# Performance work log

Measured on AMD Instinct MI355X. Metric: run time of the kernel, lower is better.

Reference implementation:

```python
import jax, jax.numpy as jnp
import numpy as np

MODEL_DIM = 1024
NUM_HEADS = 16
DIM_PER_HEAD = MODEL_DIM // NUM_HEADS
LN_EPS = 1e-5


def setup_inputs() -> dict:
    key = jax.random.key(0)
    ks = jax.random.split(key, 12)
    B, L, D = 4, 2048, MODEL_DIM
    s = 0.02
    return {
        "query": jax.random.normal(ks[0], (B, L, D), jnp.float32),
        "key": jax.random.normal(ks[1], (B, L, D), jnp.float32),
        "value": jax.random.normal(ks[2], (B, L, D), jnp.float32),
        "Wq": jax.random.normal(ks[3], (D, D), jnp.float32) * s,
        "bq": jnp.zeros((D,), jnp.float32),
        "Wk": jax.random.normal(ks[4], (D, D), jnp.float32) * s,
        "bk": jnp.zeros((D,), jnp.float32),
        "Wv": jax.random.normal(ks[5], (D, D), jnp.float32) * s,
        "bv": jnp.zeros((D,), jnp.float32),
        "Wo": jax.random.normal(ks[6], (D, D), jnp.float32) * s,
        "bo": jnp.zeros((D,), jnp.float32),
        "gamma": jnp.ones((D,), jnp.float32),
        "beta": jnp.zeros((D,), jnp.float32),
    }


def reference(query, key, value, Wq, bq, Wk, bk, Wv, bv, Wo, bo, gamma, beta):
    B, L, D = query.shape
    H, d = NUM_HEADS, DIM_PER_HEAD
    scale = d ** (-0.5)
    # torch nn.Linear: y = x @ W.T + b
    q = (query @ Wq.T + bq).reshape(B * H, L, d)  # faithful row-major view split
    k = (key @ Wk.T + bk).reshape(B * H, L, d)
    v = (value @ Wv.T + bv).reshape(B * H, L, d)
    atten = jnp.einsum('bqd,bkd->bqk', q, k) * scale  # [B*H, L, L]
    atten = jax.nn.softmax(atten, axis=2)
    # dropout: identity in eval mode
    context = jnp.einsum('bqk,bkd->bqd', atten, v).reshape(B, L, D)
    output = context @ Wo.T + bo
    x = query + output  # residual
    mu = jnp.mean(x, axis=-1, keepdims=True)
    var = jnp.var(x, axis=-1, keepdims=True)
    out = (x - mu) * jax.lax.rsqrt(var + LN_EPS) * gamma + beta
    return (out, atten)
```

## Files before the change

### kernel.cpp

```cpp
#include <hip/hip_runtime.h>
#include <cstdint>
#include <cstddef>

typedef _Float16 half8 __attribute__((ext_vector_type(8)));
typedef _Float16 half4 __attribute__((ext_vector_type(4)));
typedef __fp16 fp16x2 __attribute__((ext_vector_type(2)));
typedef float f32x4 __attribute__((ext_vector_type(4)));
typedef int int2v __attribute__((ext_vector_type(2)));

#define MFMA16(a, b, c) __builtin_amdgcn_mfma_f32_16x16x32_f16((a), (b), (c), 0, 0, 0)
#define MFMA16x16(a, b, c) __builtin_amdgcn_mfma_f32_16x16x16f16((a), (b), (c), 0, 0, 0)

__device__ __forceinline__ void gload_lds16(const void* g, void* l) {
  __builtin_amdgcn_global_load_lds(
      (const __attribute__((address_space(1))) void*)g,
      (__attribute__((address_space(3))) void*)l, 16, 0, 0);
}

__device__ __forceinline__ float fexp2(float x) {
#if __has_builtin(__builtin_amdgcn_exp2f)
  return __builtin_amdgcn_exp2f(x);
#else
  return exp2f(x);
#endif
}

__device__ __forceinline__ int cvtpk16(float a, float b) {
  fp16x2 h = __builtin_amdgcn_cvt_pkrtz(a, b);
  return __builtin_bit_cast(int, h);
}

__global__ __launch_bounds__(256) void cvt_f16(
    const float* __restrict__ q, const float* __restrict__ k, const float* __restrict__ v,
    const float* __restrict__ wq, const float* __restrict__ wk, const float* __restrict__ wv,
    _Float16* __restrict__ xq, _Float16* __restrict__ xk, _Float16* __restrict__ xv,
    _Float16* __restrict__ wq16, _Float16* __restrict__ wk16, _Float16* __restrict__ wv16)
{
  constexpr int S8 = 1048576;
  constexpr int W8 = 131072;
  int u = blockIdx.x * 256 + threadIdx.x;
  const float* src;
  _Float16* dst;
  if (u < S8) { src = q; dst = xq; }
  else if ((u -= S8) < S8) { src = k; dst = xk; }
  else if ((u -= S8) < S8) { src = v; dst = xv; }
  else if ((u -= S8) < W8) { src = wq; dst = wq16; }
  else if ((u -= W8) < W8) { src = wk; dst = wk16; }
  else { u -= W8; src = wv; dst = wv16; }
  const float4 f0 = reinterpret_cast<const float4*>(src)[u * 2];
  const float4 f1 = reinterpret_cast<const float4*>(src)[u * 2 + 1];
  half8 h;
  h[0] = (_Float16)f0.x; h[1] = (_Float16)f0.y; h[2] = (_Float16)f0.z; h[3] = (_Float16)f0.w;
  h[4] = (_Float16)f1.x; h[5] = (_Float16)f1.y; h[6] = (_Float16)f1.z; h[7] = (_Float16)f1.w;
  reinterpret_cast<half8*>(dst)[u] = h;
}

__global__ __launch_bounds__(256) void vtrans(
    const _Float16* __restrict__ v, _Float16* __restrict__ vt)
{
  __shared__ _Float16 T[64][72];
  const int g = blockIdx.y, kt = blockIdx.x;
  const int tid = threadIdx.x;
  const size_t gbase = (size_t)g * 131072;
  const int sr = tid >> 2, sc = (tid & 3) * 16;
  {
    const half8* src = reinterpret_cast<const half8*>(v + gbase + (size_t)(kt * 64 + sr) * 64 + sc);
    *reinterpret_cast<half8*>(&T[sr][sc]) = src[0];
    *reinterpret_cast<half8*>(&T[sr][sc + 8]) = src[1];
  }
  __syncthreads();
  const int d = tid >> 2, kc = (tid & 3) * 16;
  half8 h0, h1;
#pragma unroll
  for (int j = 0; j < 8; ++j) { h0[j] = T[kc + j][d]; h1[j] = T[kc + 8 + j][d]; }
  half8* dst = reinterpret_cast<half8*>(vt + gbase + (size_t)d * 2048 + kt * 64 + kc);
  dst[0] = h0;
  dst[1] = h1;
}

template <bool WF32, bool RES>
__global__ __launch_bounds__(256) void gemm128(
    const _Float16* __restrict__ A, const void* __restrict__ Wp,
    const float* __restrict__ bias, const float* __restrict__ resid,
    void* __restrict__ Out, int N, float scale)
{
  constexpr int K = 1024;
  __shared__ _Float16 As[128 * 64];
  __shared__ _Float16 Bs[128 * 64];
  const int tid = threadIdx.x;
  const int lane = tid & 63, w = tid >> 6;
  const int lo = lane & 15, hi = lane >> 4;
  const int wr = w >> 1, wc = w & 1;
  const int rbase = blockIdx.x * 128, cbase = blockIdx.y * 128;
  const int e0 = w * 512 + lane * 8;

  f32x4 acc[4][4];
#pragma unroll
  for (int m = 0; m < 4; ++m)
#pragma unroll
    for (int n = 0; n < 4; ++n) acc[m][n] = f32x4{0.f, 0.f, 0.f, 0.f};

  for (int kk = 0; kk < K; kk += 64) {
    __syncthreads();
#pragma unroll
    for (int i = 0; i < 4; ++i) {
      const int e = i * 2048 + e0;
      gload_lds16(A + (size_t)(rbase + (e >> 6)) * K + kk + (e & 63),
                  (char*)As + i * 4096 + w * 1024);
    }
    if constexpr (!WF32) {
#pragma unroll
      for (int i = 0; i < 4; ++i) {
        const int e = i * 2048 + e0;
        gload_lds16((const _Float16*)Wp + (size_t)(cbase + (e >> 6)) * K + kk + (e & 63),
                    (char*)Bs + i * 4096 + w * 1024);
      }
    } else {
#pragma unroll
      for (int i = 0; i < 4; ++i) {
        const int e = i * 2048 + e0;
        const float4* src = reinterpret_cast<const float4*>(
            (const float*)Wp + (size_t)(cbase + (e >> 6)) * K + kk + (e & 63));
        const float4 f0 = src[0], f1 = src[1];
        half8 h;
        h[0] = (_Float16)f0.x; h[1] = (_Float16)f0.y; h[2] = (_Float16)f0.z; h[3] = (_Float16)f0.w;
        h[4] = (_Float16)f1.x; h[5] = (_Float16)f1.y; h[6] = (_Float16)f1.z; h[7] = (_Float16)f1.w;
        *reinterpret_cast<half8*>(Bs + e) = h;
      }
    }
    __syncthreads();
#pragma unroll
    for (int k0 = 0; k0 < 2; ++k0) {
      half8 a[4], b[4];
#pragma unroll
      for (int m = 0; m < 4; ++m)
        a[m] = *reinterpret_cast<const half8*>(As + (wr * 64 + m * 16 + lo) * 64 + k0 * 32 + hi * 8);
#pragma unroll
      for (int n = 0; n < 4; ++n)
        b[n] = *reinterpret_cast<const half8*>(Bs + (wc * 64 + n * 16 + lo) * 64 + k0 * 32 + hi * 8);
#pragma unroll
      for (int m = 0; m < 4; ++m)
#pragma unroll
        for (int n = 0; n < 4; ++n) acc[m][n] = MFMA16(a[m], b[n], acc[m][n]);
    }
  }
#pragma unroll
  for (int m = 0; m < 4; ++m) {
#pragma unroll
    for (int n = 0; n < 4; ++n) {
      const int col = cbase + wc * 64 + n * 16 + lo;
      const float bv = bias[col];
#pragma unroll
      for (int r = 0; r < 4; ++r) {
        const int row = rbase + wr * 64 + m * 16 + hi * 4 + r;
        float v = acc[m][n][r] + bv;
        if constexpr (RES) {
          v += resid[(size_t)row * 1024 + col];
          ((float*)Out)[(size_t)row * N + col] = v;
        } else {
          ((_Float16*)Out)[(size_t)row * N + col] = (_Float16)(v * scale);
        }
      }
    }
  }
}

__global__ __launch_bounds__(512) void attn_fused(
    const _Float16* __restrict__ qg, const _Float16* __restrict__ kg,
    const _Float16* __restrict__ vtg, _Float16* __restrict__ ctx,
    float* __restrict__ attnp)
{
  __shared__ _Float16 Kt[2][64 * 64];
  __shared__ _Float16 Vt[2][64 * 64];
  __shared__ float Ps[8 * 1024];
  const int tid = threadIdx.x;
  const int lane = tid & 63, w = tid >> 6;
  const int lo = lane & 15, hi = lane >> 4;
  const int bid = blockIdx.x;
  const int g = bid & 63;
  const int q0 = (bid >> 6) * 256;
  const size_t gbase = (size_t)g * (2048 * 64);
  const int e0 = tid * 8;

  const int r0 = e0 >> 6, c0 = (e0 & 63) ^ ((r0 & 7) << 3);

  half8 q[2][2];
#pragma unroll
  for (int m = 0; m < 2; ++m)
#pragma unroll
    for (int k0 = 0; k0 < 2; ++k0)
      q[m][k0] = *reinterpret_cast<const half8*>(
          qg + gbase + (size_t)(q0 + w * 32 + m * 16 + lo) * 64 + k0 * 32 + hi * 8);

  float ls[2] = {0.f, 0.f};

  gload_lds16(kg + gbase + (size_t)r0 * 64 + c0, (char*)Kt[0] + w * 1024);

  for (int kt = 0; kt < 32; ++kt) {
    const int cur = kt & 1;
    __syncthreads();
    if (kt < 31) {
      const _Float16* kn = kg + gbase + (size_t)(kt + 1) * (64 * 64);
      gload_lds16(kn + (size_t)r0 * 64 + c0, (char*)Kt[cur ^ 1] + w * 1024);
    }
    f32x4 s[2][4];
#pragma unroll
    for (int m = 0; m < 2; ++m)
#pragma unroll
      for (int n = 0; n < 4; ++n) s[m][n] = f32x4{0.f, 0.f, 0.f, 0.f};
#pragma unroll
    for (int k0 = 0; k0 < 2; ++k0) {
      half8 b[4];
#pragma unroll
      for (int n = 0; n < 4; ++n) {
        const int row = n * 16 + lo;
        b[n] = *reinterpret_cast<const half8*>(
            Kt[cur] + row * 64 + ((k0 * 32 + hi * 8) ^ ((row & 7) << 3)));
      }
#pragma unroll
      for (int m = 0; m < 2; ++m)
#pragma unroll
        for (int n = 0; n < 4; ++n) s[m][n] = MFMA16(b[n], q[m][k0], s[m][n]);
    }
#pragma unroll
    for (int m = 0; m < 2; ++m) {
      float t = 0.f;
#pragma unroll
      for (int nb = 0; nb < 4; ++nb)
#pragma unroll
        for (int r = 0; r < 4; ++r) t += fexp2(s[m][nb][r]);
      ls[m] += t;
    }
  }

  float dr[2];
#pragma unroll
  for (int m = 0; m < 2; ++m) {
    float t = ls[m];
    t += __shfl_xor(t, 16, 64);
    t += __shfl_xor(t, 32, 64);
    dr[m] = __log2f(t);
  }

  f32x4 o[2][4];
#pragma unroll
  for (int m = 0; m < 2; ++m)
#pragma unroll
    for (int n = 0; n < 4; ++n) o[m][n] = f32x4{0.f, 0.f, 0.f, 0.f};
  float* ab = attnp + (size_t)g * 2048 * 2048;
  const _Float16* vtb = vtg + (size_t)g * (64 * 2048);

  gload_lds16(kg + gbase + (size_t)r0 * 64 + c0, (char*)Kt[0] + w * 1024);
  gload_lds16(vtb + (size_t)r0 * 2048 + c0, (char*)Vt[0] + w * 1024);

  for (int kt = 0; kt < 32; ++kt) {
    const int cur = kt & 1;
    if (kt == 0) asm volatile("s_waitcnt vmcnt(0) lgkmcnt(0)" ::: "memory");
    else asm volatile("s_waitcnt vmcnt(8) lgkmcnt(0)" ::: "memory");
    __builtin_amdgcn_s_barrier();
    __builtin_amdgcn_sched_barrier(0);
    if (kt < 31) {
      const _Float16* kn = kg + gbase + (size_t)(kt + 1) * (64 * 64);
      const _Float16* vn = vtb + (kt + 1) * 64;
      gload_lds16(kn + (size_t)r0 * 64 + c0, (char*)Kt[cur ^ 1] + w * 1024);
      gload_lds16(vn + (size_t)r0 * 2048 + c0, (char*)Vt[cur ^ 1] + w * 1024);
    }
    __builtin_amdgcn_sched_barrier(0);
    f32x4 s[2][4];
#pragma unroll
    for (int m = 0; m < 2; ++m)
#pragma unroll
      for (int n = 0; n < 4; ++n)
        s[m][n] = f32x4{-dr[m], -dr[m], -dr[m], -dr[m]};
#pragma unroll
    for (int k0 = 0; k0 < 2; ++k0) {
      half8 b[4];
#pragma unroll
      for (int n = 0; n < 4; ++n) {
        const int row = n * 16 + lo;
        b[n] = *reinterpret_cast<const half8*>(
            Kt[cur] + row * 64 + ((k0 * 32 + hi * 8) ^ ((row & 7) << 3)));
      }
#pragma unroll
      for (int m = 0; m < 2; ++m)
#pragma unroll
        for (int n = 0; n < 4; ++n) s[m][n] = MFMA16(b[n], q[m][k0], s[m][n]);
    }
    int pk[2][4][2];
    float* Pw = Ps + w * 1024;
#pragma unroll
    for (int m = 0; m < 2; ++m) {
#pragma unroll
      for (int nb = 0; nb < 4; ++nb) {
        const float p0 = fexp2(s[m][nb][0]);
        const float p1 = fexp2(s[m][nb][1]);
        const float p2 = fexp2(s[m][nb][2]);
        const float p3 = fexp2(s[m][nb][3]);
        pk[m][nb][0] = cvtpk16(p0, p1);
        pk[m][nb][1] = cvtpk16(p2, p3);
        const f32x4 f = {p0, p1, p2, p3};
        *reinterpret_cast<f32x4*>(
            Pw + lo * 64 + ((nb * 16 + hi * 4) ^ ((lo & 15) << 2))) = f;
      }
      asm volatile("s_waitcnt lgkmcnt(0)" ::: "memory");
#pragma unroll
      for (int i = 0; i < 4; ++i) {
        const int rl = i * 4 + (lane >> 4);
        const int klo = (lane & 15) * 4;
        const f32x4 f = *reinterpret_cast<const f32x4*>(
            Pw + rl * 64 + (klo ^ ((rl & 15) << 2)));
        __builtin_nontemporal_store(
            f, reinterpret_cast<f32x4*>(
                   ab + (size_t)(q0 + w * 32 + m * 16 + rl) * 2048 + kt * 64 + klo));
      }
      asm volatile("s_waitcnt lgkmcnt(0)" ::: "memory");
    }
#pragma unroll
    for (int nb = 0; nb < 4; ++nb) {
      half4 vb[4];
#pragma unroll
      for (int n = 0; n < 4; ++n) {
        const int d = n * 16 + lo;
        vb[n] = *reinterpret_cast<const half4*>(
            Vt[cur] + d * 64 + ((nb * 16 + hi * 4) ^ ((d & 7) << 3)));
      }
#pragma unroll
      for (int m = 0; m < 2; ++m) {
        const int2v t = {pk[m][nb][0], pk[m][nb][1]};
        const half4 pa = __builtin_bit_cast(half4, t);
#pragma unroll
        for (int n = 0; n < 4; ++n) o[m][n] = MFMA16x16(pa, vb[n], o[m][n]);
      }
    }
  }
#pragma unroll
  for (int m = 0; m < 2; ++m)
#pragma unroll
    for (int n = 0; n < 4; ++n)
#pragma unroll
      for (int r = 0; r < 4; ++r)
        ctx[gbase + (size_t)(q0 + w * 32 + m * 16 + hi * 4 + r) * 64 + n * 16 + lo] =
            (_Float16)o[m][n][r];
}

__global__ __launch_bounds__(256) void ln_kernel(
    float* __restrict__ x, const float* __restrict__ gamma, const float* __restrict__ beta)
{
  const int row = blockIdx.x;
  const int t = threadIdx.x;
  float4 v = *reinterpret_cast<float4*>(x + (size_t)row * 1024 + t * 4);
  float s = v.x + v.y + v.z + v.w;
  float ss = v.x * v.x + v.y * v.y + v.z * v.z + v.w * v.w;
#pragma unroll
  for (int off = 1; off < 64; off <<= 1) {
    s += __shfl_xor(s, off, 64);
    ss += __shfl_xor(ss, off, 64);
  }
  __shared__ float sm[8];
  const int wv = t >> 6, ln = t & 63;
  if (ln == 0) { sm[wv] = s; sm[4 + wv] = ss; }
  __syncthreads();
  s = sm[0] + sm[1] + sm[2] + sm[3];
  ss = sm[4] + sm[5] + sm[6] + sm[7];
  const float mu = s * (1.0f / 1024.0f);
  const float var = ss * (1.0f / 1024.0f) - mu * mu;
  const float rstd = rsqrtf(var + 1e-5f);
  const float4 gv = *reinterpret_cast<const float4*>(gamma + t * 4);
  const float4 bv = *reinterpret_cast<const float4*>(beta + t * 4);
  v.x = (v.x - mu) * rstd * gv.x + bv.x;
  v.y = (v.y - mu) * rstd * gv.y + bv.y;
  v.z = (v.z - mu) * rstd * gv.z + bv.z;
  v.w = (v.w - mu) * rstd * gv.w + bv.w;
  *reinterpret_cast<float4*>(x + (size_t)row * 1024 + t * 4) = v;
}

extern "C" void kernel_launch(void* const* d_in, const int* in_sizes, int n_in,
                              void* d_out, int out_size, void* d_ws, size_t ws_size,
                              hipStream_t stream) {
  const float* query = (const float*)d_in[0];
  const float* key_ = (const float*)d_in[1];
  const float* value = (const float*)d_in[2];
  const float* Wq = (const float*)d_in[3];
  const float* bq = (const float*)d_in[4];
  const float* Wk = (const float*)d_in[5];
  const float* bk = (const float*)d_in[6];
  const float* Wv = (const float*)d_in[7];
  const float* bv = (const float*)d_in[8];
  const float* Wo = (const float*)d_in[9];
  const float* bo = (const float*)d_in[10];
  const float* gamma = (const float*)d_in[11];
  const float* beta = (const float*)d_in[12];

  float* out = (float*)d_out;
  float* attnp = out + (size_t)8192 * 1024;

  _Float16* xq = (_Float16*)attnp;
  _Float16* xk = xq + (size_t)8388608;
  _Float16* xv = xk + (size_t)8388608;
  _Float16* wq16 = xv + (size_t)8388608;
  _Float16* wk16 = wq16 + (size_t)1048576;
  _Float16* wv16 = wk16 + (size_t)1048576;

  _Float16* vt = (_Float16*)out;

  _Float16* qb = (_Float16*)d_ws;
  _Float16* kb2 = qb + (size_t)8388608;
  _Float16* vb2 = kb2 + (size_t)8388608;
  _Float16* ctx = vb2;

  constexpr float QSCALE = 0.125f * 1.44269504088896f;

  cvt_f16<<<dim3(13824), dim3(256), 0, stream>>>(query, key_, value, Wq, Wk, Wv,
                                                 xq, xk, xv, wq16, wk16, wv16);
  gemm128<false, false><<<dim3(64, 8), dim3(256), 0, stream>>>(xq, wq16, bq, nullptr, qb, 1024, QSCALE);
  gemm128<false, false><<<dim3(64, 8), dim3(256), 0, stream>>>(xk, wk16, bk, nullptr, kb2, 1024, 1.0f);
  gemm128<false, false><<<dim3(64, 8), dim3(256), 0, stream>>>(xv, wv16, bv, nullptr, vb2, 1024, 1.0f);
  vtrans<<<dim3(32, 64), dim3(256), 0, stream>>>(vb2, vt);
  attn_fused<<<dim3(512), dim3(512), 0, stream>>>(qb, kb2, vt, ctx, attnp);
  gemm128<true, true><<<dim3(64, 8), dim3(256), 0, stream>>>(ctx, Wo, bo, query, out, 1024, 1.0f);
  ln_kernel<<<dim3(8192), dim3(256), 0, stream>>>(out, gamma, beta);
}
```

Before: 465.9 us.

## Split query tile into two halves and overlap second half's row-sum with first half's output pass

```diff
diff --git a/kernel.cpp b/kernel.cpp
--- a/kernel.cpp
+++ b/kernel.cpp
@@ -178,36 +178,36 @@
   const int lo = lane & 15, hi = lane >> 4;
   const int bid = blockIdx.x;
   const int g = bid & 63;
-  const int q0 = (bid >> 6) * 256;
+  const int qA = (bid >> 6) * 256;
+  const int qB = qA + 128;
   const size_t gbase = (size_t)g * (2048 * 64);
   const int e0 = tid * 8;
-
   const int r0 = e0 >> 6, c0 = (e0 & 63) ^ ((r0 & 7) << 3);
 
-  half8 q[2][2];
-#pragma unroll
-  for (int m = 0; m < 2; ++m)
+  float* ab = attnp + (size_t)g * 2048 * 2048;
+  const _Float16* vtb = vtg + (size_t)g * (64 * 2048);
+  float* Pw = Ps + w * 1024;
+
+  half8 qf[2][2];
+#pragma unroll
+  for (int t = 0; t < 2; ++t)
 #pragma unroll
     for (int k0 = 0; k0 < 2; ++k0)
-      q[m][k0] = *reinterpret_cast<const half8*>(
-          qg + gbase + (size_t)(q0 + w * 32 + m * 16 + lo) * 64 + k0 * 32 + hi * 8);
-
-  float ls[2] = {0.f, 0.f};
-
+      qf[t][k0] = *reinterpret_cast<const half8*>(
+          qg + gbase + (size_t)((t ? qB : qA) + w * 16 + lo) * 64 + k0 * 32 + hi * 8);
+
+  float lsA = 0.f;
   gload_lds16(kg + gbase + (size_t)r0 * 64 + c0, (char*)Kt[0] + w * 1024);
-
   for (int kt = 0; kt < 32; ++kt) {
     const int cur = kt & 1;
     __syncthreads();
     if (kt < 31) {
-      const _Float16* kn = kg + gbase + (size_t)(kt + 1) * (64 * 64);
-      gload_lds16(kn + (size_t)r0 * 64 + c0, (char*)Kt[cur ^ 1] + w * 1024);
-    }
-    f32x4 s[2][4];
-#pragma unroll
-    for (int m = 0; m < 2; ++m)
-#pragma unroll
-      for (int n = 0; n < 4; ++n) s[m][n] = f32x4{0.f, 0.f, 0.f, 0.f};
+      gload_lds16(kg + gbase + (size_t)(kt + 1) * 4096 + (size_t)r0 * 64 + c0,
+                  (char*)Kt[cur ^ 1] + w * 1024);
+    }
+    f32x4 s[4];
+#pragma unroll
+    for (int n = 0; n < 4; ++n) s[n] = f32x4{0.f, 0.f, 0.f, 0.f};
 #pragma unroll
     for (int k0 = 0; k0 < 2; ++k0) {
       half8 b[4];
@@ -218,60 +218,49 @@
             Kt[cur] + row * 64 + ((k0 * 32 + hi * 8) ^ ((row & 7) << 3)));
       }
 #pragma unroll
-      for (int m = 0; m < 2; ++m)
-#pragma unroll
-        for (int n = 0; n < 4; ++n) s[m][n] = MFMA16(b[n], q[m][k0], s[m][n]);
-    }
-#pragma unroll
-    for (int m = 0; m < 2; ++m) {
-      float t = 0.f;
-#pragma unroll
-      for (int nb = 0; nb < 4; ++nb)
-#pragma unroll
-        for (int r = 0; r < 4; ++r) t += fexp2(s[m][nb][r]);
-      ls[m] += t;
-    }
-  }
-
-  float dr[2];
-#pragma unroll
-  for (int m = 0; m < 2; ++m) {
-    float t = ls[m];
+      for (int n = 0; n < 4; ++n) s[n] = MFMA16(b[n], qf[0][k0], s[n]);
+    }
+    float t = 0.f;
+#pragma unroll
+    for (int nb = 0; nb < 4; ++nb)
+#pragma unroll
+      for (int r = 0; r < 4; ++r) t += fexp2(s[nb][r]);
+    lsA += t;
+  }
+  float drA;
+  {
+    float t = lsA;
     t += __shfl_xor(t, 16, 64);
     t += __shfl_xor(t, 32, 64);
-    dr[m] = __log2f(t);
-  }
-
-  f32x4 o[2][4];
-#pragma unroll
-  for (int m = 0; m < 2; ++m)
-#pragma unroll
-    for (int n = 0; n < 4; ++n) o[m][n] = f32x4{0.f, 0.f, 0.f, 0.f};
-  float* ab = attnp + (size_t)g * 2048 * 2048;
-  const _Float16* vtb = vtg + (size_t)g * (64 * 2048);
-
+    drA = __log2f(t);
+  }
+
+  float lsB = 0.f;
+  f32x4 o[4];
+#pragma unroll
+  for (int n = 0; n < 4; ++n) o[n] = f32x4{0.f, 0.f, 0.f, 0.f};
   gload_lds16(kg + gbase + (size_t)r0 * 64 + c0, (char*)Kt[0] + w * 1024);
   gload_lds16(vtb + (size_t)r0 * 2048 + c0, (char*)Vt[0] + w * 1024);
 
   for (int kt = 0; kt < 32; ++kt) {
     const int cur = kt & 1;
     if (kt == 0) asm volatile("s_waitcnt vmcnt(0) lgkmcnt(0)" ::: "memory");
-    else asm volatile("s_waitcnt vmcnt(8) lgkmcnt(0)" ::: "memory");
+    else asm volatile("s_waitcnt vmcnt(4) lgkmcnt(0)" ::: "memory");
     __builtin_amdgcn_s_barrier();
     __builtin_amdgcn_sched_barrier(0);
     if (kt < 31) {
-      const _Float16* kn = kg + gbase + (size_t)(kt + 1) * (64 * 64);
-      const _Float16* vn = vtb + (kt + 1) * 64;
-      gload_lds16(kn + (size_t)r0 * 64 + c0, (char*)Kt[cur ^ 1] + w * 1024);
-      gload_lds16(vn + (size_t)r0 * 2048 + c0, (char*)Vt[cur ^ 1] + w * 1024);
+      gload_lds16(kg + gbase + (size_t)(kt + 1) * 4096 + (size_t)r0 * 64 + c0,
+                  (char*)Kt[cur ^ 1] + w * 1024);
+      gload_lds16(vtb + (kt + 1) * 64 + (size_t)r0 * 2048 + c0,
+                  (char*)Vt[cur ^ 1] + w * 1024);
     }
     __builtin_amdgcn_sched_barrier(0);
-    f32x4 s[2][4];
-#pragma unroll
-    for (int m = 0; m < 2; ++m)
-#pragma unroll
-      for (int n = 0; n < 4; ++n)
-        s[m][n] = f32x4{-dr[m], -dr[m], -dr[m], -dr[m]};
+    f32x4 sA[4], sB[4];
+#pragma unroll
+    for (int n = 0; n < 4; ++n) {
+      sA[n] = f32x4{-drA, -drA, -drA, -drA};
+      sB[n] = f32x4{0.f, 0.f, 0.f, 0.f};
+    }
 #pragma unroll
     for (int k0 = 0; k0 < 2; ++k0) {
       half8 b[4];
@@ -282,38 +271,41 @@
             Kt[cur] + row * 64 + ((k0 * 32 + hi * 8) ^ ((row & 7) << 3)));
       }
 #pragma unroll
-      for (int m = 0; m < 2; ++m)
-#pragma unroll
-        for (int n = 0; n < 4; ++n) s[m][n] = MFMA16(b[n], q[m][k0], s[m][n]);
-    }
-    int pk[2][4][2];
-    float* Pw = Ps + w * 1024;
-#pragma unroll
-    for (int m = 0; m < 2; ++m) {
-#pragma unroll
-      for (int nb = 0; nb < 4; ++nb) {
-        const float p0 = fexp2(s[m][nb][0]);
-        const float p1 = fexp2(s[m][nb][1]);
-        const float p2 = fexp2(s[m][nb][2]);
-        const float p3 = fexp2(s[m][nb][3]);
-        pk[m][nb][0] = cvtpk16(p0, p1);
-        pk[m][nb][1] = cvtpk16(p2, p3);
-        const f32x4 f = {p0, p1, p2, p3};
-        *reinterpret_cast<f32x4*>(
-            Pw + lo * 64 + ((nb * 16 + hi * 4) ^ ((lo & 15) << 2))) = f;
-      }
-      asm volatile("s_waitcnt lgkmcnt(0)" ::: "memory");
-#pragma unroll
-      for (int i = 0; i < 4; ++i) {
-        const int rl = i * 4 + (lane >> 4);
-        const int klo = (lane & 15) * 4;
-        const f32x4 f = *reinterpret_cast<const f32x4*>(
-            Pw + rl * 64 + (klo ^ ((rl & 15) << 2)));
-        __builtin_nontemporal_store(
-            f, reinterpret_cast<f32x4*>(
-                   ab + (size_t)(q0 + w * 32 + m * 16 + rl) * 2048 + kt * 64 + klo));
-      }
-      asm volatile("s_waitcnt lgkmcnt(0)" ::: "memory");
+      for (int n = 0; n < 4; ++n) {
+        sA[n] = MFMA16(b[n], qf[0][k0], sA[n]);
+        sB[n] = MFMA16(b[n], qf[1][k0], sB[n]);
+      }
+    }
+    int pk[4][2];
+#pragma unroll
+    for (int nb = 0; nb < 4; ++nb) {
+      const float p0 = fexp2(sA[nb][0]);
+      const float p1 = fexp2(sA[nb][1]);
+      const float p2 = fexp2(sA[nb][2]);
+      const float p3 = fexp2(sA[nb][3]);
+      pk[nb][0] = cvtpk16(p0, p1);
+      pk[nb][1] = cvtpk16(p2, p3);
+      const f32x4 f = {p0, p1, p2, p3};
+      *reinterpret_cast<f32x4*>(Pw + lo * 64 + ((nb * 16 + hi * 4) ^ (lo << 2))) = f;
+    }
+    asm volatile("s_waitcnt lgkmcnt(0)" ::: "memory");
+#pragma unroll
+    for (int i = 0; i < 4; ++i) {
+      const int rl = i * 4 + (lane >> 4);
+      const int klo = (lane & 15) * 4;
+      const f32x4 f = *reinterpret_cast<const f32x4*>(Pw + rl * 64 + (klo ^ (rl << 2)));
+      __builtin_nontemporal_store(
+          f, reinterpret_cast<f32x4*>(
+                 ab + (size_t)(qA + w * 16 + rl) * 2048 + kt * 64 + klo));
+    }
+    asm volatile("s_waitcnt lgkmcnt(0)" ::: "memory");
+    {
+      float t = 0.f;
+#pragma unroll
+      for (int nb = 0; nb < 4; ++nb)
+#pragma unroll
+        for (int r = 0; r < 4; ++r) t += fexp2(sB[nb][r]);
+      lsB += t;
     }
 #pragma unroll
     for (int nb = 0; nb < 4; ++nb) {
@@ -324,23 +316,103 @@
         vb[n] = *reinterpret_cast<const half4*>(
             Vt[cur] + d * 64 + ((nb * 16 + hi * 4) ^ ((d & 7) << 3)));
       }
-#pragma unroll
-      for (int m = 0; m < 2; ++m) {
-        const int2v t = {pk[m][nb][0], pk[m][nb][1]};
-        const half4 pa = __builtin_bit_cast(half4, t);
-#pragma unroll
-        for (int n = 0; n < 4; ++n) o[m][n] = MFMA16x16(pa, vb[n], o[m][n]);
-      }
-    }
-  }
-#pragma unroll
-  for (int m = 0; m < 2; ++m)
-#pragma unroll
-    for (int n = 0; n < 4; ++n)
-#pragma unroll
-      for (int r = 0; r < 4; ++r)
-        ctx[gbase + (size_t)(q0 + w * 32 + m * 16 + hi * 4 + r) * 64 + n * 16 + lo] =
-            (_Float16)o[m][n][r];
+      const int2v t2 = {pk[nb][0], pk[nb][1]};
+      const half4 pa = __builtin_bit_cast(half4, t2);
+#pragma unroll
+      for (int n = 0; n < 4; ++n) o[n] = MFMA16x16(pa, vb[n], o[n]);
+    }
+  }
+#pragma unroll
+  for (int n = 0; n < 4; ++n)
+#pragma unroll
+    for (int r = 0; r < 4; ++r)
+      ctx[gbase + (size_t)(qA + w * 16 + hi * 4 + r) * 64 + n * 16 + lo] =
+          (_Float16)o[n][r];
+  float drB;
+  {
+    float t = lsB;
+    t += __shfl_xor(t, 16, 64);
+    t += __shfl_xor(t, 32, 64);
+    drB = __log2f(t);
+  }
+
+#pragma unroll
+  for (int n = 0; n < 4; ++n) o[n] = f32x4{0.f, 0.f, 0.f, 0.f};
+  gload_lds16(kg + gbase + (size_t)r0 * 64 + c0, (char*)Kt[0] + w * 1024);
+  gload_lds16(vtb + (size_t)r0 * 2048 + c0, (char*)Vt[0] + w * 1024);
+
+  for (int kt = 0; kt < 32; ++kt) {
+    const int cur = kt & 1;
+    if (kt == 0) asm volatile("s_waitcnt vmcnt(0) lgkmcnt(0)" ::: "memory");
+    else asm volatile("s_waitcnt vmcnt(4) lgkmcnt(0)" ::: "memory");
+    __builtin_amdgcn_s_barrier();
+    __builtin_amdgcn_sched_barrier(0);
+    if (kt < 31) {
+      gload_lds16(kg + gbase + (size_t)(kt + 1) * 4096 + (size_t)r0 * 64 + c0,
+                  (char*)Kt[cur ^ 1] + w * 1024);
+      gload_lds16(vtb + (kt + 1) * 64 + (size_t)r0 * 2048 + c0,
+                  (char*)Vt[cur ^ 1] + w * 1024);
+    }
+    __builtin_amdgcn_sched_barrier(0);
+    f32x4 s[4];
+#pragma unroll
+    for (int n = 0; n < 4; ++n) s[n] = f32x4{-drB, -drB, -drB, -drB};
+#pragma unroll
+    for (int k0 = 0; k0 < 2; ++k0) {
+      half8 b[4];
+#pragma unroll
+      for (int n = 0; n < 4; ++n) {
+        const int row = n * 16 + lo;
+        b[n] = *reinterpret_cast<const half8*>(
+            Kt[cur] + row * 64 + ((k0 * 32 + hi * 8) ^ ((row & 7) << 3)));
+      }
+#pragma unroll
+      for (int n = 0; n < 4; ++n) s[n] = MFMA16(b[n], qf[1][k0], s[n]);
+    }
+    int pk[4][2];
+#pragma unroll
+    for (int nb = 0; nb < 4; ++nb) {
+      const float p0 = fexp2(s[nb][0]);
+      const float p1 = fexp2(s[nb][1]);
+      const float p2 = fexp2(s[nb][2]);
+      const float p3 = fexp2(s[nb][3]);
+      pk[nb][0] = cvtpk16(p0, p1);
+      pk[nb][1] = cvtpk16(p2, p3);
+      const f32x4 f = {p0, p1, p2, p3};
+      *reinterpret_cast<f32x4*>(Pw + lo * 64 + ((nb * 16 + hi * 4) ^ (lo << 2))) = f;
+    }
+    asm volatile("s_waitcnt lgkmcnt(0)" ::: "memory");
+#pragma unroll
+    for (int i = 0; i < 4; ++i) {
+      const int rl = i * 4 + (lane >> 4);
+      const int klo = (lane & 15) * 4;
+      const f32x4 f = *reinterpret_cast<const f32x4*>(Pw + rl * 64 + (klo ^ (rl << 2)));
+      __builtin_nontemporal_store(
+          f, reinterpret_cast<f32x4*>(
+                 ab + (size_t)(qB + w * 16 + rl) * 2048 + kt * 64 + klo));
+    }
+    asm volatile("s_waitcnt lgkmcnt(0)" ::: "memory");
+#pragma unroll
+    for (int nb = 0; nb < 4; ++nb) {
+      half4 vb[4];
+#pragma unroll
+      for (int n = 0; n < 4; ++n) {
+        const int d = n * 16 + lo;
+        vb[n] = *reinterpret_cast<const half4*>(
+            Vt[cur] + d * 64 + ((nb * 16 + hi * 4) ^ ((d & 7) << 3)));
+      }
+      const int2v t2 = {pk[nb][0], pk[nb][1]};
+      const half4 pa = __builtin_bit_cast(half4, t2);
+#pragma unroll
+      for (int n = 0; n < 4; ++n) o[n] = MFMA16x16(pa, vb[n], o[n]);
+    }
+  }
+#pragma unroll
+  for (int n = 0; n < 4; ++n)
+#pragma unroll
+    for (int r = 0; r < 4; ++r)
+      ctx[gbase + (size_t)(qB + w * 16 + hi * 4 + r) * 64 + n * 16 + lo] =
+          (_Float16)o[n][r];
 }
 
 __global__ __launch_bounds__(256) void ln_kernel(
```

After: 466.4 us. About the same (+0.1%).
